# Kernel optimization log

Hardware: AMD Instinct MI355X
Metric: run time of the kernel (lower is better)

The kernel has to match this reference:

```python
import jax, jax.numpy as jnp
import numpy as np

B, C, HH, WW = 256, 1024, 7, 7
S = HH * WW            # 49 tokens
D = 1024               # hidden_size
L = 2                  # encoder_layers (nhead arg, swapped in source)
H = 2                  # attention heads (num_layers arg, swapped in source)
HD = D // H            # 512 head dim
FF = 1024              # encoder_ffn_dim
OUT = 1024             # head output
EPS = 1e-5


def setup_inputs() -> dict:
    key = jax.random.key(0)
    ks = jax.random.split(key, 10)
    n = lambda k, shape: jax.random.normal(k, shape, jnp.float32) * 0.02
    return dict(
        x=jax.random.normal(ks[0], (B, C, HH, WW), jnp.float32),
        pos_emb=n(ks[1], (S, D)),
        ln1_s=jnp.ones((L, D), jnp.float32), ln1_b=jnp.zeros((L, D), jnp.float32),
        wq=n(ks[2], (L, D, D)), wk=n(ks[3], (L, D, D)),
        wv=n(ks[4], (L, D, D)), wo=n(ks[5], (L, D, D)),
        ln2_s=jnp.ones((L, D), jnp.float32), ln2_b=jnp.zeros((L, D), jnp.float32),
        w1=n(ks[6], (L, D, FF)), b1=jnp.zeros((L, FF), jnp.float32),
        w2=n(ks[7], (L, FF, D)), b2=jnp.zeros((L, D), jnp.float32),
        lnf_s=jnp.ones((D,), jnp.float32), lnf_b=jnp.zeros((D,), jnp.float32),
        head_w=n(ks[8], (S * D, OUT)), head_b=jnp.zeros((OUT,), jnp.float32),
    )


def _ln(x, s, b):
    m = jnp.mean(x, axis=-1, keepdims=True)
    v = jnp.var(x, axis=-1, keepdims=True)
    return (x - m) * jax.lax.rsqrt(v + EPS) * s + b


def reference(x, pos_emb, ln1_s, ln1_b, wq, wk, wv, wo, ln2_s, ln2_b,
              w1, b1, w2, b2, lnf_s, lnf_b, head_w, head_b):
    b = x.shape[0]
    # flatten HxW then permute -> [B, S, D] token sequence
    h = x.reshape(b, C, S).transpose(0, 2, 1)
    # BigBirdPegasus encoder: learned pos emb added to inputs_embeds (no scaling path)
    h = h + pos_emb[None, :, :]
    scale = 1.0 / jnp.sqrt(jnp.float32(HD))
    for i in range(L):
        # --- self-attention block (pre-LN); seq_len=49 triggers original_full attention ---
        r = h
        hn = _ln(h, ln1_s[i], ln1_b[i])
        q = (hn @ wq[i]).reshape(b, S, H, HD)
        k = (hn @ wk[i]).reshape(b, S, H, HD)
        v = (hn @ wv[i]).reshape(b, S, H, HD)
        scores = jnp.einsum('bqhd,bkhd->bhqk', q, k) * scale
        attn = jax.nn.softmax(scores, axis=-1)
        ctx = jnp.einsum('bhqk,bkhd->bqhd', attn, v).reshape(b, S, D)
        h = r + ctx @ wo[i]
        # --- feed-forward block (pre-LN, gelu_new) ---
        r = h
        hn = _ln(h, ln2_s[i], ln2_b[i])
        hn = jax.nn.gelu(hn @ w1[i] + b1[i], approximate=True)
        h = r + hn @ w2[i] + b2[i]
    # BigBirdPegasus applies layernorm_embedding AFTER the layer stack
    h = _ln(h, lnf_s, lnf_b)
    # flatten + linear + relu head
    out = jax.nn.relu(h.reshape(b, S * D) @ head_w + head_b)
    return out
```

## Files before the change

### kernel.cpp

```cpp
#include <hip/hip_runtime.h>
#include <hip/hip_bf16.h>
#include <stdint.h>

#define Bq 256
#define Sq 49
#define Dq 1024
#define Hq 2
#define HDq 512
#define Mq (Bq*Sq)
#define KHEADq (Sq*Dq)
#define STq 3072

typedef unsigned short u16;
typedef short bf16x8 __attribute__((ext_vector_type(8)));
typedef float f32x4 __attribute__((ext_vector_type(4)));

__device__ inline u16 f2bf(float f){
  union { float f; uint32_t u; } c; c.f = f;
  uint32_t r = c.u + 0x7FFFu + ((c.u >> 16) & 1u);
  return (u16)(r >> 16);
}
__device__ inline float bf2f(u16 h){
  union { uint32_t u; float f; } c; c.u = ((uint32_t)h) << 16;
  return c.f;
}

#define GLOAD_LDS16(gp, lp) \
  __builtin_amdgcn_global_load_lds((__attribute__((address_space(1))) void*)(gp), \
                                   (__attribute__((address_space(3))) void*)(lp), 16, 0, 0)
#define MFMA16(a,b,c) __builtin_amdgcn_mfma_f32_16x16x32_bf16(a,b,c,0,0,0)

__global__ __launch_bounds__(256) void prep_kernel(const float* __restrict__ x,
    const float* __restrict__ pos, u16* __restrict__ h, float2* __restrict__ pstat){
  __shared__ float t[49*129];
  int b = blockIdx.x, c0 = blockIdx.y*128;
  int tid = threadIdx.x, lane = tid & 63, wave = tid >> 6;
  const float* xb = x + (size_t)b*(Dq*Sq) + (size_t)c0*Sq;
  #pragma unroll
  for(int i=0;i<32;i++){
    int cc = wave + i*4;
    if(lane < Sq) t[lane*129 + cc] = xb[(size_t)cc*Sq + lane];
  }
  __syncthreads();
  #pragma unroll
  for(int p=0;p<25;p++){
    int idx = p*256 + tid;
    int s = idx >> 7, cc = idx & 127;
    if(s < Sq){
      float hv = t[s*129 + cc] + pos[s*Dq + c0 + cc];
      h[((size_t)b*Sq + s)*Dq + c0 + cc] = f2bf(hv);
      t[s*129 + cc] = hv;
    }
  }
  __syncthreads();
  int r = tid >> 2, qd = tid & 3;
  if(r < Sq){
    float S=0.f, Q=0.f;
    for(int cc=qd; cc<128; cc+=4){ float vv = t[r*129+cc]; S+=vv; Q+=vv*vv; }
    S += __shfl_xor(S,1); Q += __shfl_xor(Q,1);
    S += __shfl_xor(S,2); Q += __shfl_xor(Q,2);
    if(qd==0){ float2 pp; pp.x=S; pp.y=Q; pstat[(size_t)blockIdx.y*Mq + b*Sq + r] = pp; }
  }
}

__global__ __launch_bounds__(256) void ln_kernel(const u16* __restrict__ hin,
    const float* __restrict__ sc, const float* __restrict__ bi, u16* __restrict__ outp){
  int wave = threadIdx.x >> 6, lane = threadIdx.x & 63;
  int row = blockIdx.x*4 + wave;
  const u16* p = hin + (size_t)row*Dq + lane*16;
  uint4 t0 = *(const uint4*)p;
  uint4 t1 = *(const uint4*)(p + 8);
  float v[16];
  {
    uint32_t wds[8] = {t0.x,t0.y,t0.z,t0.w,t1.x,t1.y,t1.z,t1.w};
    #pragma unroll
    for(int i=0;i<8;i++){
      v[2*i]   = bf2f((u16)(wds[i] & 0xffff));
      v[2*i+1] = bf2f((u16)(wds[i] >> 16));
    }
  }
  float s=0.f, sq=0.f;
  #pragma unroll
  for(int i=0;i<16;i++){ s += v[i]; sq += v[i]*v[i]; }
  #pragma unroll
  for(int o=32;o>=1;o>>=1){ s += __shfl_xor(s,o); sq += __shfl_xor(sq,o); }
  float mean = s * (1.f/Dq);
  float var  = sq * (1.f/Dq) - mean*mean;
  float rs = rsqrtf(var + 1e-5f);
  int c0 = lane*16;
  uint32_t w[8];
  #pragma unroll
  for(int i=0;i<8;i++){
    u16 lo = f2bf((v[2*i]   - mean)*rs*sc[c0+2*i]   + bi[c0+2*i]);
    u16 hi = f2bf((v[2*i+1] - mean)*rs*sc[c0+2*i+1] + bi[c0+2*i+1]);
    w[i] = (uint32_t)lo | ((uint32_t)hi << 16);
  }
  uint4* ob = (uint4*)(outp + (size_t)row*Dq + c0);
  ob[0] = make_uint4(w[0],w[1],w[2],w[3]);
  ob[1] = make_uint4(w[4],w[5],w[6],w[7]);
}

__global__ void transp_all(const float* __restrict__ wq, const float* __restrict__ wk,
    const float* __restrict__ wv, const float* __restrict__ wo,
    const float* __restrict__ w1, const float* __restrict__ w2,
    const float* __restrict__ ln1s, const float* __restrict__ ln2s, u16* __restrict__ outp){
  __shared__ float t[32][33];
  int slot = blockIdx.z; int l = slot / 6, j = slot - l*6;
  const float* srcs[6] = {wq,wk,wv,wo,w1,w2};
  const float* in = srcs[j] + (size_t)l*Dq*Dq;
  const float* sc = (j<3) ? (ln1s + l*Dq) : (j==4 ? (ln2s + l*Dq) : nullptr);
  u16* o = outp + (size_t)slot*Dq*Dq;
  int k0 = blockIdx.x*32, n0 = blockIdx.y*32;
  int tx = threadIdx.x, ty = threadIdx.y;
  #pragma unroll
  for(int i=0;i<4;i++) t[ty+8*i][tx] = in[(size_t)(k0+ty+8*i)*Dq + n0+tx];
  __syncthreads();
  float sck = sc ? sc[k0+tx] : 1.f;
  #pragma unroll
  for(int i=0;i<4;i++) o[(size_t)(n0+ty+8*i)*Dq + k0+tx] = f2bf(t[tx][ty+8*i] * sck);
}

__global__ __launch_bounds__(256) void uv_kernel(const float* __restrict__ wq,
    const float* __restrict__ wk, const float* __restrict__ wv, const float* __restrict__ w1,
    const float* __restrict__ ln1s, const float* __restrict__ ln1b,
    const float* __restrict__ ln2s, const float* __restrict__ ln2b, float* __restrict__ uvbuf){
  int bid = blockIdx.x;
  int l = bid >> 4, chunk = bid & 15;
  int col = chunk*256 + threadIdx.x;
  int j = col >> 10, n = col & 1023;
  const float* srcs[4] = {wq, wk, wv, w1};
  const float* src = srcs[j] + (size_t)l*Dq*Dq;
  const float* sc = (j<3 ? ln1s : ln2s) + l*Dq;
  const float* bi = (j<3 ? ln1b : ln2b) + l*Dq;
  float u=0.f, v=0.f;
  for(int k=0;k<Dq;k++){
    float val = src[(size_t)k*Dq + n];
    u += sc[k]*val; v += bi[k]*val;
  }
  uvbuf[((size_t)l*4096 + col)*2]   = u;
  uvbuf[((size_t)l*4096 + col)*2+1] = v;
}

template<int EPI>
__global__ __launch_bounds__(512, 2) void gemm_nt2(
    const u16* __restrict__ A, int lda,
    const u16* __restrict__ Bt, int ldb,
    void* __restrict__ Cout, const u16* __restrict__ resid,
    const float* __restrict__ bias, int ldc,
    const float2* __restrict__ pstat_in, int nchunk,
    const float* __restrict__ uvp, float2* __restrict__ pstat_out)
{
  __shared__ u16 lds[65536];
  int tid = threadIdx.x, lane = tid & 63;
  int wave = tid >> 6;
  int wm = wave >> 2, wn = wave & 3;
  int l15 = lane & 15, l4 = lane >> 4;
  int swz = (l15 & 7) << 4;

  int gx = gridDim.x, nwg = gx*gridDim.y;
  int orig = blockIdx.y*gx + blockIdx.x;
  int qq = nwg >> 3, rr = nwg & 7;
  int xcd = orig & 7, idx = orig >> 3;
  int wgid = (xcd < rr ? xcd*(qq+1) : rr*(qq+1) + (xcd-rr)*qq) + idx;
  int bx = wgid % gx, by = wgid / gx;
  int m0 = by*256, n0 = bx*256;

  int srow = tid >> 3, scolb = (tid & 7) * 16;
  int scolx = scolb ^ ((srow & 7) << 4);
  auto stage2 = [&](int d, int kt, int h){
    #pragma unroll
    for(int cc=0; cc<2; cc++){
      int c = 2*h + cc;
      if(c < 4){
        int row = c*64 + srow;
        const u16* src = A + (size_t)(m0+row)*lda + kt*64 + (scolx>>1);
        GLOAD_LDS16(src, &lds[d*16384 + c*4096 + tid*8]);
      } else {
        int c4 = c - 4;
        int row = c4*64 + srow;
        const u16* src = Bt + (size_t)(n0+row)*ldb + kt*64 + (scolx>>1);
        GLOAD_LDS16(src, &lds[32768 + d*16384 + c4*4096 + tid*8]);
      }
    }
  };
  auto rdA = [&](int d, int i, int s)->bf16x8{
    int row = wm*128 + i*16 + l15;
    int byt = row*128 + ((s*64 + l4*16) ^ swz);
    return *(const bf16x8*)((const char*)lds + d*32768 + byt);
  };
  auto rdB = [&](int d, int n, int s)->bf16x8{
    int row = wn*64 + n*16 + l15;
    int byt = row*128 + ((s*64 + l4*16) ^ swz);
    return *(const bf16x8*)((const char*)lds + 65536 + d*32768 + byt);
  };

  f32x4 acc[8][4] = {};

  #pragma unroll
  for(int h=0;h<4;h++) stage2(0, 0, h);

  for(int t=0; t<16; ++t){
    int d = t & 1;
    bf16x8 bfr[4][2];
    if(t < 15){
      stage2(d^1, t+1, 0);
      asm volatile("s_waitcnt vmcnt(2)" ::: "memory");
    } else {
      asm volatile("s_waitcnt vmcnt(0)" ::: "memory");
    }
    __builtin_amdgcn_sched_barrier(0);
    __builtin_amdgcn_s_barrier();
    bfr[0][0]=rdB(d,0,0); bfr[0][1]=rdB(d,0,1);
    bfr[1][0]=rdB(d,1,0); bfr[1][1]=rdB(d,1,1);
    bf16x8 a0s0=rdA(d,0,0), a0s1=rdA(d,0,1), a1s0=rdA(d,1,0), a1s1=rdA(d,1,1);
    __builtin_amdgcn_s_setprio(1);
    acc[0][0]=MFMA16(a0s0,bfr[0][0],acc[0][0]); acc[0][0]=MFMA16(a0s1,bfr[0][1],acc[0][0]);
    acc[0][1]=MFMA16(a0s0,bfr[1][0],acc[0][1]); acc[0][1]=MFMA16(a0s1,bfr[1][1],acc[0][1]);
    acc[1][0]=MFMA16(a1s0,bfr[0][0],acc[1][0]); acc[1][0]=MFMA16(a1s1,bfr[0][1],acc[1][0]);
    acc[1][1]=MFMA16(a1s0,bfr[1][0],acc[1][1]); acc[1][1]=MFMA16(a1s1,bfr[1][1],acc[1][1]);
    __builtin_amdgcn_s_setprio(0);
    __builtin_amdgcn_s_barrier();
    bfr[2][0]=rdB(d,2,0); bfr[2][1]=rdB(d,2,1);
    bfr[3][0]=rdB(d,3,0); bfr[3][1]=rdB(d,3,1);
    if(t < 15) stage2(d^1, t+1, 1);
    __builtin_amdgcn_s_barrier();
    __builtin_amdgcn_s_setprio(1);
    acc[0][2]=MFMA16(a0s0,bfr[2][0],acc[0][2]); acc[0][2]=MFMA16(a0s1,bfr[2][1],acc[0][2]);
    acc[0][3]=MFMA16(a0s0,bfr[3][0],acc[0][3]); acc[0][3]=MFMA16(a0s1,bfr[3][1],acc[0][3]);
    acc[1][2]=MFMA16(a1s0,bfr[2][0],acc[1][2]); acc[1][2]=MFMA16(a1s1,bfr[2][1],acc[1][2]);
    acc[1][3]=MFMA16(a1s0,bfr[3][0],acc[1][3]); acc[1][3]=MFMA16(a1s1,bfr[3][1],acc[1][3]);
    __builtin_amdgcn_s_setprio(0);
    __builtin_amdgcn_s_barrier();
    #pragma unroll
    for(int q=1;q<4;q++){
      bf16x8 c0s0=rdA(d,2*q,0), c0s1=rdA(d,2*q,1), c1s0=rdA(d,2*q+1,0), c1s1=rdA(d,2*q+1,1);
      if(t < 15 && q < 3) stage2(d^1, t+1, q+1);
      __builtin_amdgcn_s_barrier();
      __builtin_amdgcn_s_setprio(1);
      #pragma unroll
      for(int n=0;n<4;n++){
        acc[2*q][n]   = MFMA16(c0s0, bfr[n][0], acc[2*q][n]);
        acc[2*q][n]   = MFMA16(c0s1, bfr[n][1], acc[2*q][n]);
        acc[2*q+1][n] = MFMA16(c1s0, bfr[n][0], acc[2*q+1][n]);
        acc[2*q+1][n] = MFMA16(c1s1, bfr[n][1], acc[2*q+1][n]);
      }
      __builtin_amdgcn_s_setprio(0);
      __builtin_amdgcn_s_barrier();
    }
  }

  if constexpr (EPI == 1){
    float2* statsS = (float2*)((char*)lds + 49152);
    float* slotf = (float*)((char*)lds + wave*4096);
    float bv[4];
    #pragma unroll
    for(int n=0;n<4;n++) bv[n] = bias ? bias[n0 + wn*64 + n*16 + l15] : 0.f;
    #pragma unroll
    for(int i=0;i<8;i++){
      #pragma unroll
      for(int n=0;n<4;n++)
        #pragma unroll
        for(int r=0;r<4;r++)
          slotf[(l4*4+r)*64 + n*16 + l15] = acc[i][n][r] + bv[n];
      #pragma unroll
      for(int st=0;st<2;st++){
        int u = st*64 + lane;
        int row = u >> 3, c8 = (u & 7)*8;
        f32x4 lo = *(const f32x4*)&slotf[row*64 + c8];
        f32x4 hi = *(const f32x4*)&slotf[row*64 + c8 + 4];
        size_t o = (size_t)(m0 + wm*128 + i*16 + row)*ldc + n0 + wn*64 + c8;
        bf16x8 rb = *(const bf16x8*)(resid + o);
        bf16x8 ov; float fs=0.f, fq=0.f;
        #pragma unroll
        for(int j=0;j<4;j++){
          float a_ = lo[j] + bf2f((u16)rb[j]);
          float b_ = hi[j] + bf2f((u16)rb[4+j]);
          ov[j]   = (short)f2bf(a_);
          ov[4+j] = (short)f2bf(b_);
          fs += a_ + b_; fq += a_*a_ + b_*b_;
        }
        *(bf16x8*)((u16*)Cout + o) = ov;
        fs += __shfl_xor(fs,1); fq += __shfl_xor(fq,1);
        fs += __shfl_xor(fs,2); fq += __shfl_xor(fq,2);
        fs += __shfl_xor(fs,4); fq += __shfl_xor(fq,4);
        if((lane&7)==0){
          float2 pp; pp.x=fs; pp.y=fq;
          statsS[(wm*128 + i*16 + st*8 + (lane>>3))*4 + wn] = pp;
        }
      }
    }
    __syncthreads();
    if(tid < 256){
      float S=0.f, Q=0.f;
      #pragma unroll
      for(int w2_=0;w2_<4;w2_++){ float2 pp = statsS[tid*4+w2_]; S+=pp.x; Q+=pp.y; }
      float2 pp; pp.x=S; pp.y=Q;
      pstat_out[(size_t)bx*Mq + m0 + tid] = pp;
    }
  } else {
    float2* lstat = (float2*)((char*)lds + 49152);
    if(tid < 256){
      float S=0.f, Q=0.f;
      for(int c=0;c<nchunk;c++){ float2 pp = pstat_in[(size_t)c*Mq + m0 + tid]; S+=pp.x; Q+=pp.y; }
      float mean = S*(1.f/1024.f);
      float var  = Q*(1.f/1024.f) - mean*mean;
      float2 sm; sm.x = rsqrtf(var + 1e-5f); sm.y = mean;
      lstat[tid] = sm;
    }
    __syncthreads();
    u16* slot = (u16*)((char*)lds + wave*2048);
    float uvv[4][2], bv[4];
    #pragma unroll
    for(int n=0;n<4;n++){
      int ncol = n0 + wn*64 + n*16 + l15;
      float2 uv2 = ((const float2*)uvp)[ncol];
      uvv[n][0] = uv2.x; uvv[n][1] = uv2.y;
      if constexpr (EPI == 2) bv[n] = bias[ncol];
    }
    #pragma unroll
    for(int i=0;i<8;i++){
      #pragma unroll
      for(int n=0;n<4;n++)
        #pragma unroll
        for(int r=0;r<4;r++){
          float2 sm = lstat[wm*128 + i*16 + l4*4 + r];
          float va = sm.x*acc[i][n][r] - sm.x*sm.y*uvv[n][0] + uvv[n][1];
          u16 ov;
          if constexpr (EPI == 0){
            ov = f2bf(va);
          } else {
            float xg = va + bv[n];
            float tg = tanhf(0.79788456080286536f*(xg + 0.044715f*xg*xg*xg));
            ov = f2bf(0.5f*xg*(1.f+tg));
          }
          slot[(l4*4+r)*64 + n*16 + l15] = ov;
        }
      #pragma unroll
      for(int st=0;st<2;st++){
        int u = st*64 + lane;
        int row = u >> 3, c8 = (u & 7)*8;
        bf16x8 v8 = *(const bf16x8*)&slot[row*64 + c8];
        *(bf16x8*)((u16*)Cout + (size_t)(m0 + wm*128 + i*16 + row)*ldc + n0 + wn*64 + c8) = v8;
      }
    }
  }
}

__global__ __launch_bounds__(256) void gemm_head(
    const u16* __restrict__ A, const float* __restrict__ W,
    float* __restrict__ parts)
{
  __shared__ u16 sA[128*32];
  __shared__ float sC[4][1024];
  int tid = threadIdx.x, lane = tid & 63;
  int wave = tid >> 6;
  int wm = wave >> 1, wn = wave & 1;
  int l15 = lane & 15, l4 = lane >> 4;
  int nwg = gridDim.x*gridDim.y*gridDim.z;
  int orig = (blockIdx.z*gridDim.y + blockIdx.y)*gridDim.x + blockIdx.x;
  int cpx = nwg >> 3;
  int swz = (orig & 7)*cpx + (orig >> 3);
  int bx = swz & 7, by = (swz >> 3) & 1, z = swz >> 4;
  int m0 = by*128, n0 = bx*128;
  size_t abase = (size_t)m0*KHEADq + (size_t)z*1024;
  f32x4 acc[4][4] = {};
  const float* wp = W + ((size_t)z*1024 + (size_t)l4*8)*1024 + n0 + wn*64 + l15;
  for(int kt=0;kt<32;kt++){
    #pragma unroll
    for(int c=0;c<2;c++){
      int s2 = c*256+tid;
      GLOAD_LDS16(A + abase + (size_t)(s2>>2)*KHEADq + kt*32 + (s2&3)*8, &sA[s2*8]);
    }
    float wreg[4][8];
    #pragma unroll
    for(int f=0;f<4;f++)
      #pragma unroll
      for(int jj=0;jj<8;jj++)
        wreg[f][jj] = wp[(size_t)(kt*32+jj)*1024 + f*16];
    bf16x8 bfr[4];
    #pragma unroll
    for(int f=0;f<4;f++){
      bf16x8 bv;
      #pragma unroll
      for(int jj=0;jj<8;jj++)
        bv[jj] = __builtin_bit_cast(short, __float2bfloat16(wreg[f][jj]));
      bfr[f] = bv;
    }
    __syncthreads();
    bf16x8 af[4];
    #pragma unroll
    for(int f=0;f<4;f++)
      af[f] = *(const bf16x8*)&sA[(wm*64 + f*16 + l15)*32 + l4*8];
    #pragma unroll
    for(int i=0;i<4;i++)
      #pragma unroll
      for(int j=0;j<4;j++)
        acc[i][j] = MFMA16(af[i], bfr[j], acc[i][j]);
    __syncthreads();
  }
  float* base = parts + (size_t)z*(Bq*1024);
  #pragma unroll
  for(int i=0;i<4;i++){
    #pragma unroll
    for(int j=0;j<4;j++)
      #pragma unroll
      for(int r=0;r<4;r++)
        sC[wave][(l4*4+r)*64 + j*16 + l15] = acc[i][j][r];
    #pragma unroll
    for(int st=0;st<4;st++){
      int u = st*64 + lane;
      int row = u >> 4, c4 = (u & 15)*4;
      f32x4 v4 = *(const f32x4*)&sC[wave][row*64 + c4];
      *(f32x4*)(base + (size_t)(m0+wm*64+i*16+row)*1024 + n0+wn*64+c4) = v4;
    }
  }
}

__global__ __launch_bounds__(256) void attn_kernel(u16* __restrict__ qkv)
{
  __shared__ float sS[64][65];
  __shared__ u16 sP[64][64];
  int bh = blockIdx.x;
  int b = bh >> 1, h = bh & 1;
  int tid = threadIdx.x, lane = tid & 63, wave = tid >> 6;
  int l15 = lane & 15, l4 = lane >> 4;
  f32x4 zero4 = {0.f,0.f,0.f,0.f};
  bf16x8 zb = {0,0,0,0,0,0,0,0};
  f32x4 acc[4];
  #pragma unroll
  for(int i=0;i<4;i++) acc[i] = zero4;
  int srow = wave*16 + l15;
  const u16* qp = qkv + (size_t)(b*Sq + srow)*STq + h*HDq + l4*8;
  const u16* kbase = qkv + (size_t)b*Sq*STq + Dq + h*HDq + l4*8;
  for(int kt=0;kt<16;kt++){
    bf16x8 aq = (srow < Sq) ? *(const bf16x8*)(qp + kt*32) : zb;
    #pragma unroll
    for(int fn=0;fn<4;fn++){
      int s2 = fn*16 + l15;
      bf16x8 bk = (s2 < Sq) ? *(const bf16x8*)(kbase + (size_t)s2*STq + kt*32) : zb;
      acc[fn] = MFMA16(aq, bk, acc[fn]);
    }
  }
  const float scale = 0.04419417382415922f;
  #pragma unroll
  for(int fn=0;fn<4;fn++)
    #pragma unroll
    for(int r=0;r<4;r++)
      sS[wave*16 + l4*4 + r][fn*16 + l15] = acc[fn][r]*scale;
  __syncthreads();
  {
    int r = tid >> 2, qd = tid & 3;
    float mx = -1e30f;
    for(int j=qd;j<Sq;j+=4) mx = fmaxf(mx, sS[r][j]);
    mx = fmaxf(mx, __shfl_xor(mx,1));
    mx = fmaxf(mx, __shfl_xor(mx,2));
    float sum = 0.f;
    for(int j=qd;j<Sq;j+=4){ float e = __expf(sS[r][j]-mx); sS[r][j]=e; sum+=e; }
    sum += __shfl_xor(sum,1);
    sum += __shfl_xor(sum,2);
    float inv = 1.f/sum;
    for(int j=qd;j<64;j+=4) sP[r][j] = (j<Sq)? f2bf(sS[r][j]*inv) : (u16)0;
  }
  __syncthreads();
  bf16x8 ap[2];
  #pragma unroll
  for(int kt2=0;kt2<2;kt2++)
    ap[kt2] = *(const bf16x8*)&sP[wave*16 + l15][kt2*32 + l4*8];
  const u16* vbp = qkv + (size_t)b*Sq*STq + 2*Dq + h*HDq + l15;
  u16* cb = qkv + (size_t)b*Sq*STq + h*HDq;
  for(int fn=0;fn<32;fn++){
    f32x4 c4 = zero4;
    #pragma unroll
    for(int kt2=0;kt2<2;kt2++){
      const u16* vp = vbp + fn*16 + (size_t)(kt2*32 + l4*8)*STq;
      bf16x8 bv;
      #pragma unroll
      for(int jj=0;jj<8;jj++) bv[jj] = (short)vp[(size_t)jj*STq];
      c4 = MFMA16(ap[kt2], bv, c4);
    }
    #pragma unroll
    for(int r=0;r<4;r++){
      int s = wave*16 + l4*4 + r;
      if(s < Sq) cb[(size_t)s*STq + fn*16 + l15] = f2bf(c4[r]);
    }
  }
}

__global__ __launch_bounds__(256) void head_finalize(const float* __restrict__ parts,
    const float* __restrict__ hb, float* __restrict__ outp){
  int idx = blockIdx.x*256 + threadIdx.x;
  float s = hb[idx & 1023];
  #pragma unroll
  for(int z=0;z<49;z++) s += parts[(size_t)z*(Bq*1024) + idx];
  outp[idx] = fmaxf(s, 0.f);
}

extern "C" void kernel_launch(void* const* d_in, const int* in_sizes, int n_in,
                              void* d_out, int out_size, void* d_ws, size_t ws_size,
                              hipStream_t stream) {
  (void)in_sizes; (void)n_in; (void)out_size;
  const float* x    = (const float*)d_in[0];
  const float* pos  = (const float*)d_in[1];
  const float* ln1s = (const float*)d_in[2];
  const float* ln1b = (const float*)d_in[3];
  const float* wq   = (const float*)d_in[4];
  const float* wk   = (const float*)d_in[5];
  const float* wv   = (const float*)d_in[6];
  const float* wo   = (const float*)d_in[7];
  const float* ln2s = (const float*)d_in[8];
  const float* ln2b = (const float*)d_in[9];
  const float* w1   = (const float*)d_in[10];
  const float* b1   = (const float*)d_in[11];
  const float* w2   = (const float*)d_in[12];
  const float* b2   = (const float*)d_in[13];
  const float* lnfs = (const float*)d_in[14];
  const float* lnfb = (const float*)d_in[15];
  const float* hw   = (const float*)d_in[16];
  const float* hb   = (const float*)d_in[17];
  float* out = (float*)d_out;

  char* ws = (char*)d_ws;
  size_t off = 0;
  auto carve = [&](size_t n) -> char* { char* p = ws + off; off += (n + 255) & ~(size_t)255; return p; };
  u16*   h     = (u16*)  carve((size_t)Mq*Dq*2);
  u16*   act0  = (u16*)  carve((size_t)Mq*Dq*2);
  u16*   act1  = (u16*)  carve((size_t)Mq*Dq*2);
  u16*   qkv   = (u16*)  carve((size_t)(Mq+16)*STq*2);
  u16*   wT    = (u16*)  carve((size_t)12*Dq*Dq*2);
  float2* pstat= (float2*)carve((size_t)8*Mq*sizeof(float2));
  float* uvbuf = (float*)carve((size_t)2*4096*2*4);
  float* parts = (float*)qkv;
  if (off > ws_size) return;

  hipMemsetAsync(qkv + (size_t)Mq*STq, 0, (size_t)16*STq*2, stream);

  prep_kernel<<<dim3(Bq, 8), 256, 0, stream>>>(x, pos, h, pstat);
  transp_all<<<dim3(32,32,12), dim3(32,8), 0, stream>>>(wq, wk, wv, wo, w1, w2, ln1s, ln2s, wT);
  uv_kernel<<<32, 256, 0, stream>>>(wq, wk, wv, w1, ln1s, ln1b, ln2s, ln2b, uvbuf);

  dim3 gg(4, Mq/256);
  dim3 gq(12, Mq/256);
  for(int l=0;l<2;l++){
    u16* qkvT = wT + (size_t)(l*6+0)*Dq*Dq;
    u16* woT  = wT + (size_t)(l*6+3)*Dq*Dq;
    u16* w1T  = wT + (size_t)(l*6+4)*Dq*Dq;
    u16* w2T  = wT + (size_t)(l*6+5)*Dq*Dq;
    const float* uvq = uvbuf + (size_t)l*8192;
    const float* uv1 = uvbuf + (size_t)l*8192 + 3072*2;

    gemm_nt2<0><<<gq, 512, 0, stream>>>(h, Dq, qkvT, Dq, qkv, nullptr, nullptr, STq,
                                        pstat, (l==0)?8:4, uvq, nullptr);
    attn_kernel<<<Bq*Hq, 256, 0, stream>>>(qkv);
    gemm_nt2<1><<<gg, 512, 0, stream>>>(qkv, STq, woT, Dq, h, h, nullptr, Dq,
                                        nullptr, 0, nullptr, pstat);
    gemm_nt2<2><<<gg, 512, 0, stream>>>(h, Dq, w1T, Dq, act1, nullptr, b1 + l*Dq, Dq,
                                        pstat, 4, uv1, nullptr);
    gemm_nt2<1><<<gg, 512, 0, stream>>>(act1, Dq, w2T, Dq, h, h, b2 + l*Dq, Dq,
                                        nullptr, 0, nullptr, pstat);
  }

  ln_kernel<<<Mq/4, 256, 0, stream>>>(h, lnfs, lnfb, act0);
  gemm_head<<<dim3(8,2,49), 256, 0, stream>>>(act0, hw, parts);
  head_finalize<<<1024, 256, 0, stream>>>(parts, hb, out);
}
```

Before: 742.1 us.

## Rework head GEMM tiling, bf16 partials, parallel uv reduction, fold memset

The head GEMM now covers all 256 rows per block, so each fp32 head weight tile is read and converted once instead of twice. Its blocks are mapped so each XCD column owns whole z-slices. Split-K partials are stored as bf16 rather than fp32, halving partial-sum write and read traffic at some precision cost in the 49-way reduction. The uv column reduction is split across 8 k-slices per column with a shared-memory reduce, raising parallelism from 32 blocks to 256. The padding memset is folded into prep_kernel to drop one launch.

```diff
diff --git a/kernel.cpp b/kernel.cpp
--- a/kernel.cpp
+++ b/kernel.cpp
@@ -31,10 +31,17 @@
 #define MFMA16(a,b,c) __builtin_amdgcn_mfma_f32_16x16x32_bf16(a,b,c,0,0,0)
 
 __global__ __launch_bounds__(256) void prep_kernel(const float* __restrict__ x,
-    const float* __restrict__ pos, u16* __restrict__ h, float2* __restrict__ pstat){
+    const float* __restrict__ pos, u16* __restrict__ h, float2* __restrict__ pstat,
+    u16* __restrict__ qkv){
   __shared__ float t[49*129];
   int b = blockIdx.x, c0 = blockIdx.y*128;
   int tid = threadIdx.x, lane = tid & 63, wave = tid >> 6;
+  if(b == 0){
+    uint4* pz = (uint4*)(qkv + (size_t)Mq*STq + (size_t)blockIdx.y*6144);
+    pz[tid] = make_uint4(0,0,0,0);
+    pz[256+tid] = make_uint4(0,0,0,0);
+    pz[512+tid] = make_uint4(0,0,0,0);
+  }
   const float* xb = x + (size_t)b*(Dq*Sq) + (size_t)c0*Sq;
   #pragma unroll
   for(int i=0;i<32;i++){
@@ -120,25 +127,35 @@
   for(int i=0;i<4;i++) o[(size_t)(n0+ty+8*i)*Dq + k0+tx] = f2bf(t[tx][ty+8*i] * sck);
 }
 
-__global__ __launch_bounds__(256) void uv_kernel(const float* __restrict__ wq,
+__global__ __launch_bounds__(256) void uv_all_kernel(const float* __restrict__ wq,
     const float* __restrict__ wk, const float* __restrict__ wv, const float* __restrict__ w1,
     const float* __restrict__ ln1s, const float* __restrict__ ln1b,
     const float* __restrict__ ln2s, const float* __restrict__ ln2b, float* __restrict__ uvbuf){
-  int bid = blockIdx.x;
-  int l = bid >> 4, chunk = bid & 15;
-  int col = chunk*256 + threadIdx.x;
+  __shared__ float2 red[8][32];
+  int t = threadIdx.x;
+  int colg = blockIdx.x*32 + (t & 31);
+  int ks = t >> 5;
+  int l = colg >> 12, col = colg & 4095;
   int j = col >> 10, n = col & 1023;
   const float* srcs[4] = {wq, wk, wv, w1};
   const float* src = srcs[j] + (size_t)l*Dq*Dq;
   const float* sc = (j<3 ? ln1s : ln2s) + l*Dq;
   const float* bi = (j<3 ? ln1b : ln2b) + l*Dq;
   float u=0.f, v=0.f;
-  for(int k=0;k<Dq;k++){
+  for(int k=ks*128;k<ks*128+128;k++){
     float val = src[(size_t)k*Dq + n];
     u += sc[k]*val; v += bi[k]*val;
   }
-  uvbuf[((size_t)l*4096 + col)*2]   = u;
-  uvbuf[((size_t)l*4096 + col)*2+1] = v;
+  float2 pp; pp.x=u; pp.y=v;
+  red[ks][t&31] = pp;
+  __syncthreads();
+  if(t < 32){
+    float U=0.f, V=0.f;
+    #pragma unroll
+    for(int s2=0;s2<8;s2++){ float2 q2 = red[s2][t]; U+=q2.x; V+=q2.y; }
+    uvbuf[(size_t)(blockIdx.x*32 + t)*2]   = U;
+    uvbuf[(size_t)(blockIdx.x*32 + t)*2+1] = V;
+  }
 }
 
 template<int EPI>
@@ -348,70 +365,67 @@
 
 __global__ __launch_bounds__(256) void gemm_head(
     const u16* __restrict__ A, const float* __restrict__ W,
-    float* __restrict__ parts)
+    u16* __restrict__ parts)
 {
-  __shared__ u16 sA[128*32];
-  __shared__ float sC[4][1024];
+  __shared__ u16 sA[256*32];
   int tid = threadIdx.x, lane = tid & 63;
   int wave = tid >> 6;
   int wm = wave >> 1, wn = wave & 1;
   int l15 = lane & 15, l4 = lane >> 4;
-  int nwg = gridDim.x*gridDim.y*gridDim.z;
-  int orig = (blockIdx.z*gridDim.y + blockIdx.y)*gridDim.x + blockIdx.x;
-  int cpx = nwg >> 3;
-  int swz = (orig & 7)*cpx + (orig >> 3);
-  int bx = swz & 7, by = (swz >> 3) & 1, z = swz >> 4;
-  int m0 = by*128, n0 = bx*128;
-  size_t abase = (size_t)m0*KHEADq + (size_t)z*1024;
-  f32x4 acc[4][4] = {};
+  int c = blockIdx.x, r = blockIdx.y;
+  int nz = (c==0) ? 7 : 6;
+  int bx = r / nz;
+  if(bx >= 8) return;
+  int z = c + 8*(r - bx*nz);
+  int n0 = bx*128;
+  f32x4 acc[8][4] = {};
   const float* wp = W + ((size_t)z*1024 + (size_t)l4*8)*1024 + n0 + wn*64 + l15;
   for(int kt=0;kt<32;kt++){
     #pragma unroll
-    for(int c=0;c<2;c++){
-      int s2 = c*256+tid;
-      GLOAD_LDS16(A + abase + (size_t)(s2>>2)*KHEADq + kt*32 + (s2&3)*8, &sA[s2*8]);
-    }
-    float wreg[4][8];
-    #pragma unroll
-    for(int f=0;f<4;f++)
+    for(int cc=0;cc<4;cc++){
+      int s2 = cc*256+tid;
+      GLOAD_LDS16(A + (size_t)(s2>>2)*KHEADq + (size_t)z*1024 + kt*32 + (s2&3)*8, &sA[s2*8]);
+    }
+    bf16x8 bfr[4];
+    #pragma unroll
+    for(int f=0;f<4;f++){
+      float wreg[8];
       #pragma unroll
       for(int jj=0;jj<8;jj++)
-        wreg[f][jj] = wp[(size_t)(kt*32+jj)*1024 + f*16];
-    bf16x8 bfr[4];
-    #pragma unroll
-    for(int f=0;f<4;f++){
+        wreg[jj] = wp[(size_t)(kt*32+jj)*1024 + f*16];
       bf16x8 bv;
       #pragma unroll
       for(int jj=0;jj<8;jj++)
-        bv[jj] = __builtin_bit_cast(short, __float2bfloat16(wreg[f][jj]));
+        bv[jj] = __builtin_bit_cast(short, __float2bfloat16(wreg[jj]));
       bfr[f] = bv;
     }
     __syncthreads();
-    bf16x8 af[4];
-    #pragma unroll
-    for(int f=0;f<4;f++)
-      af[f] = *(const bf16x8*)&sA[(wm*64 + f*16 + l15)*32 + l4*8];
-    #pragma unroll
-    for(int i=0;i<4;i++)
+    bf16x8 af[8];
+    #pragma unroll
+    for(int i=0;i<8;i++)
+      af[i] = *(const bf16x8*)&sA[(wm*128 + i*16 + l15)*32 + l4*8];
+    #pragma unroll
+    for(int i=0;i<8;i++)
       #pragma unroll
       for(int j=0;j<4;j++)
         acc[i][j] = MFMA16(af[i], bfr[j], acc[i][j]);
     __syncthreads();
   }
-  float* base = parts + (size_t)z*(Bq*1024);
-  #pragma unroll
-  for(int i=0;i<4;i++){
+  u16* slot = &sA[wave*2048];
+  u16* base = parts + (size_t)z*(Bq*1024);
+  #pragma unroll
+  for(int i=0;i<8;i++){
     #pragma unroll
     for(int j=0;j<4;j++)
       #pragma unroll
-      for(int r=0;r<4;r++)
-        sC[wave][(l4*4+r)*64 + j*16 + l15] = acc[i][j][r];
-    #pragma unroll
-    for(int st=0;st<4;st++){
+      for(int rr=0;rr<4;rr++)
+        slot[(l4*4+rr)*64 + j*16 + l15] = f2bf(acc[i][j][rr]);
+    #pragma unroll
+    for(int st=0;st<2;st++){
       int u = st*64 + lane;
-      int row = u >> 4, c4 = (u & 15)*4;
-      f32x4 v4 = *(const f32x4*)&sC[wave][row*64 + c4];
-      *(f32x4*)(base + (size_t)(m0+wm*64+i*16+row)*1024 + n0+wn*64+c4) = v4;
+      int row = u >> 3, c8 = (u & 7)*8;
+      bf16x8 v8 = *(const bf16x8*)&slot[row*64 + c8];
+      *(bf16x8*)(base + (size_t)(wm*128 + i*16 + row)*1024 + n0 + wn*64 + c8) = v8;
     }
   }
 }
@@ -486,12 +500,12 @@
   }
 }
 
-__global__ __launch_bounds__(256) void head_finalize(const float* __restrict__ parts,
+__global__ __launch_bounds__(256) void head_finalize(const u16* __restrict__ parts,
     const float* __restrict__ hb, float* __restrict__ outp){
   int idx = blockIdx.x*256 + threadIdx.x;
   float s = hb[idx & 1023];
   #pragma unroll
-  for(int z=0;z<49;z++) s += parts[(size_t)z*(Bq*1024) + idx];
+  for(int z=0;z<49;z++) s += bf2f(parts[(size_t)z*(Bq*1024) + idx]);
   outp[idx] = fmaxf(s, 0.f);
 }
 
@@ -529,14 +543,12 @@
   u16*   wT    = (u16*)  carve((size_t)12*Dq*Dq*2);
   float2* pstat= (float2*)carve((size_t)8*Mq*sizeof(float2));
   float* uvbuf = (float*)carve((size_t)2*4096*2*4);
-  float* parts = (float*)qkv;
+  u16*   parts = qkv;
   if (off > ws_size) return;
 
-  hipMemsetAsync(qkv + (size_t)Mq*STq, 0, (size_t)16*STq*2, stream);
-
-  prep_kernel<<<dim3(Bq, 8), 256, 0, stream>>>(x, pos, h, pstat);
+  prep_kernel<<<dim3(Bq, 8), 256, 0, stream>>>(x, pos, h, pstat, qkv);
   transp_all<<<dim3(32,32,12), dim3(32,8), 0, stream>>>(wq, wk, wv, wo, w1, w2, ln1s, ln2s, wT);
-  uv_kernel<<<32, 256, 0, stream>>>(wq, wk, wv, w1, ln1s, ln1b, ln2s, ln2b, uvbuf);
+  uv_all_kernel<<<256, 256, 0, stream>>>(wq, wk, wv, w1, ln1s, ln1b, ln2s, ln2b, uvbuf);
 
   dim3 gg(4, Mq/256);
   dim3 gq(12, Mq/256);
@@ -560,6 +572,6 @@
   }
 
   ln_kernel<<<Mq/4, 256, 0, stream>>>(h, lnfs, lnfb, act0);
-  gemm_head<<<dim3(8,2,49), 256, 0, stream>>>(act0, hw, parts);
+  gemm_head<<<dim3(8,56), 256, 0, stream>>>(act0, hw, parts);
   head_finalize<<<1024, 256, 0, stream>>>(parts, hb, out);
 }
```

Result: faster. 692.0 us (-6.8%).
